# Performance work log

Hardware: AMD Instinct MI355X
Metric: run time of the kernel (lower is better)

## Reference

```python
import jax, jax.numpy as jnp
import numpy as np

B, D, C = 2048, 1024, 8192


def setup_inputs() -> dict:
    key = jax.random.key(0)
    k1, k2, k3 = jax.random.split(key, 3)
    x = jax.random.normal(k1, (B, D), dtype=jnp.float32)
    y = jax.random.randint(k2, (B,), 0, C)
    centroids = jax.random.normal(k3, (C, D), dtype=jnp.float32)
    return {"x": x, "y": y, "centroids": centroids}


def reference(x, y, centroids):
    x2 = jnp.sum(x * x, axis=-1, keepdims=True)          # (B, 1)
    c2 = jnp.sum(centroids * centroids, axis=-1)          # (C,)
    logits = -(x2 + c2[None, :] - 2.0 * (x @ centroids.T))  # (B, C)
    decisions = jnp.argmax(logits, axis=1)                # nearest centroid
    score = jnp.mean((decisions == y).astype(jnp.float32))
    # CrossEntropyLoss(distances, y)
    logp = jax.nn.log_softmax(logits, axis=-1)
    loss = -jnp.mean(jnp.take_along_axis(logp, y[:, None], axis=1))
    return loss, score
```

## Files before the change

### kernel.cpp

```cpp
#include <hip/hip_runtime.h>
#include <cstdint>

#define MDIM 2048
#define KDIM 1024
#define CDIM 8192
#define BM 256
#define BN 256
#define BK 32
#define NT (KDIM / BK)
#define NCHUNK (CDIM / 64)

typedef __attribute__((ext_vector_type(8))) __bf16 bf16x8;
typedef __attribute__((ext_vector_type(4))) float f32x4;

__device__ __forceinline__ unsigned short f2bf(float f) {
  unsigned u = __float_as_uint(f);
  u += 0x7fffu + ((u >> 16) & 1u);
  return (unsigned short)(u >> 16);
}

__device__ __forceinline__ void async_ld16(const void* g, void* l) {
  __builtin_amdgcn_global_load_lds(
      (__attribute__((address_space(1))) void*)(g),
      (__attribute__((address_space(3))) void*)(l),
      16, 0, 0);
}

__global__ __launch_bounds__(256) void convert_all(const float* __restrict__ x,
                                                   const float* __restrict__ cent,
                                                   unsigned short* __restrict__ xb,
                                                   unsigned short* __restrict__ cb,
                                                   float* __restrict__ c2) {
  const int b = blockIdx.x, t = threadIdx.x;
  if (b < MDIM) {
    const float4 v = ((const float4*)(x + (size_t)b * KDIM))[t];
    ushort4 o;
    o.x = f2bf(v.x); o.y = f2bf(v.y); o.z = f2bf(v.z); o.w = f2bf(v.w);
    ((ushort4*)(xb + (size_t)b * KDIM))[t] = o;
  } else {
    const int row = b - MDIM;
    const float4 v = ((const float4*)(cent + (size_t)row * KDIM))[t];
    ushort4 o;
    o.x = f2bf(v.x); o.y = f2bf(v.y); o.z = f2bf(v.z); o.w = f2bf(v.w);
    ((ushort4*)(cb + (size_t)row * KDIM))[t] = o;
    float p = v.x * v.x + v.y * v.y + v.z * v.z + v.w * v.w;
    for (int d = 32; d; d >>= 1) p += __shfl_down(p, d, 64);
    __shared__ float red[4];
    if ((t & 63) == 0) red[t >> 6] = p;
    __syncthreads();
    if (t == 0) c2[row] = red[0] + red[1] + red[2] + red[3];
  }
}

__global__ __launch_bounds__(512, 2) void gemm_reduce(
    const unsigned short* __restrict__ Ab, const unsigned short* __restrict__ Bb,
    const float* __restrict__ c2,
    float* __restrict__ pm, float* __restrict__ pl, int* __restrict__ pidx) {
  __shared__ __align__(16) char lds[4 * 32768];

  const int tid = threadIdx.x;
  const int wave = tid >> 6, lane = tid & 63;
  const int wm = wave >> 2, wn = wave & 3;
  const int quad = lane >> 4, c16 = lane & 15;

  const int id = blockIdx.y * gridDim.x + blockIdx.x;
  const int lid = (id & 7) * 32 + (id >> 3);
  const int bm = lid >> 5, bn = lid & 31;
  const int bmBase = bm * BM, bnBase = bn * BN;

  const int r1 = tid >> 2, c1 = (tid & 3) ^ ((r1 >> 1) & 3);
  const int r2 = (tid + 512) >> 2, c2s = (tid & 3) ^ ((r2 >> 1) & 3);
  const char* Ag1 = (const char*)(Ab + (size_t)(bmBase + r1) * KDIM + c1 * 8);
  const char* Ag2 = (const char*)(Ab + (size_t)(bmBase + r2) * KDIM + c2s * 8);
  const char* Bg1 = (const char*)(Bb + (size_t)(bnBase + r1) * KDIM + c1 * 8);
  const char* Bg2 = (const char*)(Bb + (size_t)(bnBase + r2) * KDIM + c2s * 8);
  const int wbyte = wave * 1024;

  int aoff[8], boff[4];
#pragma unroll
  for (int mt = 0; mt < 8; ++mt) {
    const int row = wm * 128 + mt * 16 + c16;
    aoff[mt] = row * 64 + ((quad ^ ((row >> 1) & 3)) * 16);
  }
#pragma unroll
  for (int nt = 0; nt < 4; ++nt) {
    const int col = wn * 64 + nt * 16 + c16;
    boff[nt] = col * 64 + ((quad ^ ((col >> 1) & 3)) * 16);
  }

  f32x4 acc[8][4] = {};

#define STAGE(T)                                          \
  {                                                       \
    const int _ko = (T) * (BK * 2);                       \
    char* _sb = &lds[((T) & 3) * 32768];                  \
    async_ld16(Ag1 + _ko, _sb + wbyte);                   \
    async_ld16(Ag2 + _ko, _sb + 8192 + wbyte);            \
    async_ld16(Bg1 + _ko, _sb + 16384 + wbyte);           \
    async_ld16(Bg2 + _ko, _sb + 24576 + wbyte);           \
  }

  STAGE(0); STAGE(1); STAGE(2);

#pragma unroll 1
  for (int t = 0; t < NT; ++t) {
    if (t < NT - 2)       asm volatile("s_waitcnt vmcnt(8)" ::: "memory");
    else if (t == NT - 2) asm volatile("s_waitcnt vmcnt(4)" ::: "memory");
    else                  asm volatile("s_waitcnt vmcnt(0)" ::: "memory");
    __builtin_amdgcn_s_barrier();
    __builtin_amdgcn_sched_barrier(0);

    const char* sb = &lds[(t & 3) * 32768];
    bf16x8 a[8], b[4];
#pragma unroll
    for (int mt = 0; mt < 8; ++mt) a[mt] = *(const bf16x8*)(sb + aoff[mt]);
#pragma unroll
    for (int nt = 0; nt < 4; ++nt) b[nt] = *(const bf16x8*)(sb + 16384 + boff[nt]);

    if (t < NT - 3) STAGE(t + 3);

    asm volatile("s_waitcnt lgkmcnt(0)" ::: "memory");
    __builtin_amdgcn_sched_barrier(0);
    __builtin_amdgcn_s_setprio(1);
#pragma unroll
    for (int mt = 0; mt < 8; ++mt)
#pragma unroll
      for (int nt = 0; nt < 4; ++nt)
        acc[mt][nt] = __builtin_amdgcn_mfma_f32_16x16x32_bf16(a[mt], b[nt], acc[mt][nt], 0, 0, 0);
    __builtin_amdgcn_s_setprio(0);
  }
#undef STAGE

  const int colbase = bnBase + wn * 64;
  float c2v[4];
#pragma unroll
  for (int nt = 0; nt < 4; ++nt) c2v[nt] = c2[colbase + nt * 16 + c16];

  const int chunk = bn * 4 + wn;
#pragma unroll
  for (int mt = 0; mt < 8; ++mt) {
#pragma unroll
    for (int r = 0; r < 4; ++r) {
      float sv[4];
#pragma unroll
      for (int nt = 0; nt < 4; ++nt) sv[nt] = 2.0f * acc[mt][nt][r] - c2v[nt];
      float m = sv[0];
      int idx = colbase + c16;
#pragma unroll
      for (int nt = 1; nt < 4; ++nt) {
        if (sv[nt] > m) { m = sv[nt]; idx = colbase + nt * 16 + c16; }
      }
      float l = 0.f;
#pragma unroll
      for (int nt = 0; nt < 4; ++nt) l += __expf(sv[nt] - m);
      for (int d = 1; d < 16; d <<= 1) {
        float om = __shfl_xor(m, d, 64);
        float ol = __shfl_xor(l, d, 64);
        int oi = __shfl_xor(idx, d, 64);
        float M = fmaxf(m, om);
        l = l * __expf(m - M) + ol * __expf(om - M);
        idx = (om > m || (om == m && oi < idx)) ? oi : idx;
        m = M;
      }
      if (c16 == 0) {
        const int row = bmBase + wm * 128 + mt * 16 + quad * 4 + r;
        pm[(size_t)row * NCHUNK + chunk] = m;
        pl[(size_t)row * NCHUNK + chunk] = l;
        pidx[(size_t)row * NCHUNK + chunk] = idx;
      }
    }
  }
}

__global__ __launch_bounds__(128) void combine_kernel(
    const float* __restrict__ pm, const float* __restrict__ pl,
    const int* __restrict__ pidx, const float* __restrict__ x,
    const float* __restrict__ cent, const float* __restrict__ c2,
    const int* __restrict__ y,
    float* __restrict__ loss_part, float* __restrict__ corr_part) {
  const int row = blockIdx.x, t = threadIdx.x;
  const int yc = y[row];

  float m = pm[(size_t)row * NCHUNK + t];
  float l = pl[(size_t)row * NCHUNK + t];
  int idx = pidx[(size_t)row * NCHUNK + t];

  const float4* xa = (const float4*)(x + (size_t)row * KDIM) + t * 2;
  const float4* ca = (const float4*)(cent + (size_t)yc * KDIM) + t * 2;
  const float4 a0 = xa[0], a1 = xa[1], b0 = ca[0], b1 = ca[1];
  float dot = a0.x * b0.x + a0.y * b0.y + a0.z * b0.z + a0.w * b0.w
            + a1.x * b1.x + a1.y * b1.y + a1.z * b1.z + a1.w * b1.w;

  for (int d = 1; d < 64; d <<= 1) {
    const float om = __shfl_xor(m, d, 64);
    const float ol = __shfl_xor(l, d, 64);
    const int oi = __shfl_xor(idx, d, 64);
    const float od = __shfl_xor(dot, d, 64);
    const float M = fmaxf(m, om);
    l = l * __expf(m - M) + ol * __expf(om - M);
    idx = (om > m || (om == m && oi < idx)) ? oi : idx;
    m = M;
    dot += od;
  }
  __shared__ float sm[2], sl[2], sd[2];
  __shared__ int si[2];
  if ((t & 63) == 0) { sm[t >> 6] = m; sl[t >> 6] = l; si[t >> 6] = idx; sd[t >> 6] = dot; }
  __syncthreads();
  if (t == 0) {
    const float m0 = sm[0], m1 = sm[1];
    const float M = fmaxf(m0, m1);
    const float L = sl[0] * __expf(m0 - M) + sl[1] * __expf(m1 - M);
    int g;
    if (m1 > m0 || (m1 == m0 && si[1] < si[0])) g = si[1]; else g = si[0];
    const float sy = 2.0f * (sd[0] + sd[1]) - c2[yc];
    loss_part[row] = __logf(L) + M - sy;
    corr_part[row] = (g == yc) ? 1.f : 0.f;
  }
}

__global__ __launch_bounds__(256) void finalize(const float* __restrict__ loss_part,
                                                const float* __restrict__ corr_part,
                                                float* __restrict__ out) {
  const int t = threadIdx.x;
  float s0 = 0.f, s1 = 0.f;
  for (int i = t; i < MDIM; i += 256) { s0 += loss_part[i]; s1 += corr_part[i]; }
  for (int d = 32; d; d >>= 1) {
    s0 += __shfl_down(s0, d, 64);
    s1 += __shfl_down(s1, d, 64);
  }
  __shared__ float r0[4], r1[4];
  if ((t & 63) == 0) { r0[t >> 6] = s0; r1[t >> 6] = s1; }
  __syncthreads();
  if (t == 0) {
    out[0] = (r0[0] + r0[1] + r0[2] + r0[3]) * (1.0f / MDIM);
    out[1] = (r1[0] + r1[1] + r1[2] + r1[3]) * (1.0f / MDIM);
  }
}

extern "C" void kernel_launch(void* const* d_in, const int* in_sizes, int n_in,
                              void* d_out, int out_size, void* d_ws, size_t ws_size,
                              hipStream_t stream) {
  const float* x = (const float*)d_in[0];
  const int* y = (const int*)d_in[1];
  const float* cent = (const float*)d_in[2];
  float* out = (float*)d_out;

  char* ws = (char*)d_ws;
  const size_t OFF_XB = 0;
  const size_t OFF_CB = OFF_XB + (size_t)MDIM * KDIM * 2;
  const size_t OFF_C2 = OFF_CB + (size_t)CDIM * KDIM * 2;
  const size_t OFF_PM = OFF_C2 + (size_t)CDIM * 4;
  const size_t OFF_PL = OFF_PM + (size_t)NCHUNK * MDIM * 4;
  const size_t OFF_PI = OFF_PL + (size_t)NCHUNK * MDIM * 4;
  const size_t OFF_LP = OFF_PI + (size_t)NCHUNK * MDIM * 4;
  const size_t OFF_CP = OFF_LP + (size_t)MDIM * 4;
  const size_t NEED = OFF_CP + (size_t)MDIM * 4;
  if (ws_size < NEED) return;

  unsigned short* xb = (unsigned short*)(ws + OFF_XB);
  unsigned short* cb = (unsigned short*)(ws + OFF_CB);
  float* c2 = (float*)(ws + OFF_C2);
  float* pm = (float*)(ws + OFF_PM);
  float* pl = (float*)(ws + OFF_PL);
  int* pidx = (int*)(ws + OFF_PI);
  float* loss_part = (float*)(ws + OFF_LP);
  float* corr_part = (float*)(ws + OFF_CP);

  convert_all<<<MDIM + CDIM, 256, 0, stream>>>(x, cent, xb, cb, c2);
  gemm_reduce<<<dim3(CDIM / BN, MDIM / BM), 512, 0, stream>>>(xb, cb, c2, pm, pl, pidx);
  combine_kernel<<<MDIM, 128, 0, stream>>>(pm, pl, pidx, x, cent, c2, y, loss_part, corr_part);
  finalize<<<1, 256, 0, stream>>>(loss_part, corr_part, out);
}
```

Baseline: 138.3 us.

## Split main-loop into two half-phases interleaving A/B prefetch with MFMA

```diff
diff --git a/kernel.cpp b/kernel.cpp
--- a/kernel.cpp
+++ b/kernel.cpp
@@ -90,7 +90,7 @@
 
   f32x4 acc[8][4] = {};
 
-#define STAGE(T)                                          \
+#define STAGE_FULL(T)                                     \
   {                                                       \
     const int _ko = (T) * (BK * 2);                       \
     char* _sb = &lds[((T) & 3) * 32768];                  \
@@ -100,36 +100,67 @@
     async_ld16(Bg2 + _ko, _sb + 24576 + wbyte);           \
   }
 
-  STAGE(0); STAGE(1); STAGE(2);
+  STAGE_FULL(0); STAGE_FULL(1); STAGE_FULL(2);
+  asm volatile("s_waitcnt vmcnt(8)" ::: "memory");
+  __builtin_amdgcn_s_barrier();
+  __builtin_amdgcn_sched_barrier(0);
 
 #pragma unroll 1
   for (int t = 0; t < NT; ++t) {
-    if (t < NT - 2)       asm volatile("s_waitcnt vmcnt(8)" ::: "memory");
-    else if (t == NT - 2) asm volatile("s_waitcnt vmcnt(4)" ::: "memory");
-    else                  asm volatile("s_waitcnt vmcnt(0)" ::: "memory");
+    const char* sb = &lds[(t & 3) * 32768];
+    bf16x8 a0[4], a1[4], b[4];
+
+#pragma unroll
+    for (int mt = 0; mt < 4; ++mt) a0[mt] = *(const bf16x8*)(sb + aoff[mt]);
+#pragma unroll
+    for (int nt = 0; nt < 4; ++nt) b[nt] = *(const bf16x8*)(sb + 16384 + boff[nt]);
+    if (t < NT - 3) {
+      const int ko = (t + 3) * (BK * 2);
+      char* db = &lds[((t + 3) & 3) * 32768];
+      async_ld16(Ag1 + ko, db + wbyte);
+      async_ld16(Ag2 + ko, db + 8192 + wbyte);
+    }
     __builtin_amdgcn_s_barrier();
-    __builtin_amdgcn_sched_barrier(0);
-
-    const char* sb = &lds[(t & 3) * 32768];
-    bf16x8 a[8], b[4];
-#pragma unroll
-    for (int mt = 0; mt < 8; ++mt) a[mt] = *(const bf16x8*)(sb + aoff[mt]);
-#pragma unroll
-    for (int nt = 0; nt < 4; ++nt) b[nt] = *(const bf16x8*)(sb + 16384 + boff[nt]);
-
-    if (t < NT - 3) STAGE(t + 3);
-
     asm volatile("s_waitcnt lgkmcnt(0)" ::: "memory");
     __builtin_amdgcn_sched_barrier(0);
     __builtin_amdgcn_s_setprio(1);
 #pragma unroll
-    for (int mt = 0; mt < 8; ++mt)
+    for (int mt = 0; mt < 4; ++mt)
 #pragma unroll
       for (int nt = 0; nt < 4; ++nt)
-        acc[mt][nt] = __builtin_amdgcn_mfma_f32_16x16x32_bf16(a[mt], b[nt], acc[mt][nt], 0, 0, 0);
+        acc[mt][nt] = __builtin_amdgcn_mfma_f32_16x16x32_bf16(a0[mt], b[nt], acc[mt][nt], 0, 0, 0);
     __builtin_amdgcn_s_setprio(0);
-  }
-#undef STAGE
+    __builtin_amdgcn_s_barrier();
+    __builtin_amdgcn_sched_barrier(0);
+
+#pragma unroll
+    for (int mt = 0; mt < 4; ++mt) a1[mt] = *(const bf16x8*)(sb + aoff[4 + mt]);
+    if (t < NT - 3) {
+      const int ko = (t + 3) * (BK * 2);
+      char* db = &lds[((t + 3) & 3) * 32768];
+      async_ld16(Bg1 + ko, db + 16384 + wbyte);
+      async_ld16(Bg2 + ko, db + 24576 + wbyte);
+    }
+    __builtin_amdgcn_s_barrier();
+    asm volatile("s_waitcnt lgkmcnt(0)" ::: "memory");
+    __builtin_amdgcn_sched_barrier(0);
+    __builtin_amdgcn_s_setprio(1);
+#pragma unroll
+    for (int mt = 0; mt < 4; ++mt)
+#pragma unroll
+      for (int nt = 0; nt < 4; ++nt)
+        acc[4 + mt][nt] = __builtin_amdgcn_mfma_f32_16x16x32_bf16(a1[mt], b[nt], acc[4 + mt][nt], 0, 0, 0);
+    __builtin_amdgcn_s_setprio(0);
+
+    if (t < NT - 1) {
+      if (t <= NT - 4)      asm volatile("s_waitcnt vmcnt(8)" ::: "memory");
+      else if (t == NT - 3) asm volatile("s_waitcnt vmcnt(4)" ::: "memory");
+      else                  asm volatile("s_waitcnt vmcnt(0)" ::: "memory");
+      __builtin_amdgcn_s_barrier();
+      __builtin_amdgcn_sched_barrier(0);
+    }
+  }
+#undef STAGE_FULL
 
   const int colbase = bnBase + wn * 64;
   float c2v[4];
```

Measured after the change: 138.8 us. About the same (+0.3%).

## Unroll K-loop by two and interleave LDS fragment reads with MFMA halves

Applied to the files above, without the earlier changes.

```diff
diff --git a/kernel.cpp b/kernel.cpp
--- a/kernel.cpp
+++ b/kernel.cpp
@@ -103,30 +103,69 @@
   STAGE(0); STAGE(1); STAGE(2);
 
 #pragma unroll 1
-  for (int t = 0; t < NT; ++t) {
-    if (t < NT - 2)       asm volatile("s_waitcnt vmcnt(8)" ::: "memory");
-    else if (t == NT - 2) asm volatile("s_waitcnt vmcnt(4)" ::: "memory");
-    else                  asm volatile("s_waitcnt vmcnt(0)" ::: "memory");
+  for (int i = 0; i < NT / 2; ++i) {
+    const int t0 = 2 * i;
+    const char* sbE = &lds[(t0 & 3) * 32768];
+    const char* sbO = &lds[((t0 + 1) & 3) * 32768];
+
+    if (i == NT / 2 - 1) asm volatile("s_waitcnt vmcnt(0)" ::: "memory");
+    else                 asm volatile("s_waitcnt vmcnt(4)" ::: "memory");
     __builtin_amdgcn_s_barrier();
     __builtin_amdgcn_sched_barrier(0);
 
-    const char* sb = &lds[(t & 3) * 32768];
-    bf16x8 a[8], b[4];
-#pragma unroll
-    for (int mt = 0; mt < 8; ++mt) a[mt] = *(const bf16x8*)(sb + aoff[mt]);
-#pragma unroll
-    for (int nt = 0; nt < 4; ++nt) b[nt] = *(const bf16x8*)(sb + 16384 + boff[nt]);
-
-    if (t < NT - 3) STAGE(t + 3);
-
+    bf16x8 aE[8], bE[4], aO[8], bO[4];
+#pragma unroll
+    for (int mt = 0; mt < 4; ++mt) aE[mt] = *(const bf16x8*)(sbE + aoff[mt]);
+#pragma unroll
+    for (int nt = 0; nt < 4; ++nt) bE[nt] = *(const bf16x8*)(sbE + 16384 + boff[nt]);
+#pragma unroll
+    for (int mt = 4; mt < 8; ++mt) aE[mt] = *(const bf16x8*)(sbE + aoff[mt]);
+    if (t0 + 3 < NT) STAGE(t0 + 3);
+    asm volatile("s_waitcnt lgkmcnt(4)" ::: "memory");
+    __builtin_amdgcn_sched_barrier(0);
+    __builtin_amdgcn_s_setprio(1);
+#pragma unroll
+    for (int mt = 0; mt < 4; ++mt)
+#pragma unroll
+      for (int nt = 0; nt < 4; ++nt)
+        acc[mt][nt] = __builtin_amdgcn_mfma_f32_16x16x32_bf16(aE[mt], bE[nt], acc[mt][nt], 0, 0, 0);
+    __builtin_amdgcn_s_setprio(0);
     asm volatile("s_waitcnt lgkmcnt(0)" ::: "memory");
     __builtin_amdgcn_sched_barrier(0);
+    __builtin_amdgcn_s_barrier();
+
+#pragma unroll
+    for (int mt = 0; mt < 4; ++mt) aO[mt] = *(const bf16x8*)(sbO + aoff[mt]);
+#pragma unroll
+    for (int nt = 0; nt < 4; ++nt) bO[nt] = *(const bf16x8*)(sbO + 16384 + boff[nt]);
+    if (t0 + 4 < NT) STAGE(t0 + 4);
+    __builtin_amdgcn_sched_barrier(0);
     __builtin_amdgcn_s_setprio(1);
 #pragma unroll
-    for (int mt = 0; mt < 8; ++mt)
+    for (int mt = 4; mt < 8; ++mt)
 #pragma unroll
       for (int nt = 0; nt < 4; ++nt)
-        acc[mt][nt] = __builtin_amdgcn_mfma_f32_16x16x32_bf16(a[mt], b[nt], acc[mt][nt], 0, 0, 0);
+        acc[mt][nt] = __builtin_amdgcn_mfma_f32_16x16x32_bf16(aE[mt], bE[nt], acc[mt][nt], 0, 0, 0);
+    __builtin_amdgcn_s_setprio(0);
+#pragma unroll
+    for (int mt = 4; mt < 8; ++mt) aO[mt] = *(const bf16x8*)(sbO + aoff[mt]);
+    asm volatile("s_waitcnt lgkmcnt(4)" ::: "memory");
+    __builtin_amdgcn_sched_barrier(0);
+    __builtin_amdgcn_s_setprio(1);
+#pragma unroll
+    for (int mt = 0; mt < 4; ++mt)
+#pragma unroll
+      for (int nt = 0; nt < 4; ++nt)
+        acc[mt][nt] = __builtin_amdgcn_mfma_f32_16x16x32_bf16(aO[mt], bO[nt], acc[mt][nt], 0, 0, 0);
+    __builtin_amdgcn_s_setprio(0);
+    asm volatile("s_waitcnt lgkmcnt(0)" ::: "memory");
+    __builtin_amdgcn_sched_barrier(0);
+    __builtin_amdgcn_s_setprio(1);
+#pragma unroll
+    for (int mt = 4; mt < 8; ++mt)
+#pragma unroll
+      for (int nt = 0; nt < 4; ++nt)
+        acc[mt][nt] = __builtin_amdgcn_mfma_f32_16x16x32_bf16(aO[mt], bO[nt], acc[mt][nt], 0, 0, 0);
     __builtin_amdgcn_s_setprio(0);
   }
 #undef STAGE
```

Measured after the change: 135.8 us. Within noise of the previous version (-1.8%).
